# Kernel tuning notes

Hardware: AMD Instinct MI355X
Metric: run time of the kernel (lower is better)

The kernel has to match this reference:

```python
import jax, jax.numpy as jnp
import numpy as np

N = 100_000      # n_nodes
E = 1_000_000    # n_edges (avg degree 10)
DIN = 64
DOUT = 64


def setup_inputs() -> dict:
    key = jax.random.key(0)
    k1, k2, k3, k4 = jax.random.split(key, 4)
    x = jax.random.normal(k1, (N, DIN), dtype=jnp.float32)
    edge_index = jax.random.randint(k2, (2, E), 0, N, dtype=jnp.int32)
    # GCNConv linear weight (glorot-ish scale) and bias
    W = jax.random.normal(k3, (DIN, DOUT), dtype=jnp.float32) * (1.0 / np.sqrt(DIN))
    b = jax.random.normal(k4, (DOUT,), dtype=jnp.float32) * 0.01
    return {"x": x, "edge_index": edge_index, "W": W, "b": b}


def reference(x, edge_index, W, b):
    n = x.shape[0]
    # linear transform first (PyG GCNConv: x = self.lin(x))
    h = x @ W  # [N, DOUT]
    # add self-loops
    loop = jnp.arange(n, dtype=edge_index.dtype)
    row = jnp.concatenate([edge_index[0], loop])  # source j
    col = jnp.concatenate([edge_index[1], loop])  # target i
    # symmetric normalization: deg computed on target index (PyG gcn_norm)
    deg = jax.ops.segment_sum(jnp.ones(row.shape[0], dtype=h.dtype), col, num_segments=n)
    dinv = jnp.where(deg > 0, jax.lax.rsqrt(deg), 0.0)
    norm = dinv[row] * dinv[col]  # [E+N]
    # gather source features, scale, scatter-add to targets
    out = jax.ops.segment_sum(norm[:, None] * h[row], col, num_segments=n)
    out = out + b
    # dropout is identity in eval mode; act = relu
    return jax.nn.relu(out)
```

## Files before the change

kernel.cpp:

```cpp
#include <hip/hip_runtime.h>
#include <hip/hip_bf16.h>

#define F 64
#define BK 128
#define CAP 4096
#define ECAP 2048
#define PA_BLOCKS 256

typedef __attribute__((ext_vector_type(8))) short bf16x8;
typedef __attribute__((ext_vector_type(4))) float f32x4;

static __device__ inline short f2bf_bits(float f) {
    union { __hip_bfloat16 b; short s; } cv;
    cv.b = __float2bfloat16(f);
    return cv.s;
}

__global__ void __launch_bounds__(256)
passA_kernel(const int* __restrict__ row, const int* __restrict__ col,
             int* __restrict__ bcursor, unsigned* __restrict__ bin,
             int e, int K, int chunk) {
    __shared__ int lh[1024];
    __shared__ int lbase[1024];
    int tid = threadIdx.x;
    int s = blockIdx.x * chunk;
    int lim = min(s + chunk, e);
    for (int i = tid; i < K; i += 256) lh[i] = 0;
    __syncthreads();
    for (int i = s + tid; i < lim; i += 256) atomicAdd(&lh[col[i] >> 7], 1);
    __syncthreads();
    for (int i = tid; i < K; i += 256) {
        int c = lh[i];
        lbase[i] = c ? atomicAdd(&bcursor[i], c) : 0;
        lh[i] = 0;
    }
    __syncthreads();
    for (int i = s + tid; i < lim; i += 256) {
        int d = col[i];
        int bkt = d >> 7;
        int off = lbase[bkt] + atomicAdd(&lh[bkt], 1);
        if (off < CAP)
            bin[(size_t)bkt * CAP + off] = ((unsigned)row[i] << 7) | ((unsigned)d & 127u);
    }
}

__global__ void __launch_bounds__(256)
k2_kernel(const float* __restrict__ x, const float* __restrict__ W,
          __hip_bfloat16* __restrict__ h,
          const unsigned* __restrict__ bin, const int* __restrict__ bcursor,
          float* __restrict__ dinv, int n, int ngemm) {
    __shared__ short Wb[F * F];
    __shared__ int lcnt[BK];
    int tid = threadIdx.x;

    if ((int)blockIdx.x < ngemm) {
        for (int i = tid; i < F * F; i += 256) Wb[i] = f2bf_bits(W[i]);
        __syncthreads();
        int lane = tid & 63;
        int wv = tid >> 6;
        int quad = lane >> 4;
        int l16 = lane & 15;

        bf16x8 bfr[2][4];
#pragma unroll
        for (int ks = 0; ks < 2; ++ks)
#pragma unroll
            for (int nb = 0; nb < 4; ++nb) {
                bf16x8 f;
#pragma unroll
                for (int j = 0; j < 8; ++j)
                    f[j] = Wb[(ks * 32 + quad * 8 + j) * F + nb * 16 + l16];
                bfr[ks][nb] = f;
            }

        int blockbase = blockIdx.x * 256;
#pragma unroll
        for (int mt = 0; mt < 4; ++mt) {
            int trow = blockbase + (wv * 4 + mt) * 16;
            int ar = trow + l16;
            bf16x8 af0, af1;
            if (ar < n) {
                const float* xr = x + (size_t)ar * F + quad * 8;
                float4 v0 = ((const float4*)xr)[0];
                float4 v1 = ((const float4*)xr)[1];
                float4 v2 = ((const float4*)(xr + 32))[0];
                float4 v3 = ((const float4*)(xr + 32))[1];
                af0[0] = f2bf_bits(v0.x); af0[1] = f2bf_bits(v0.y);
                af0[2] = f2bf_bits(v0.z); af0[3] = f2bf_bits(v0.w);
                af0[4] = f2bf_bits(v1.x); af0[5] = f2bf_bits(v1.y);
                af0[6] = f2bf_bits(v1.z); af0[7] = f2bf_bits(v1.w);
                af1[0] = f2bf_bits(v2.x); af1[1] = f2bf_bits(v2.y);
                af1[2] = f2bf_bits(v2.z); af1[3] = f2bf_bits(v2.w);
                af1[4] = f2bf_bits(v3.x); af1[5] = f2bf_bits(v3.y);
                af1[6] = f2bf_bits(v3.z); af1[7] = f2bf_bits(v3.w);
            } else {
                af0 = (bf16x8)0; af1 = (bf16x8)0;
            }
            f32x4 acc[4];
#pragma unroll
            for (int nb = 0; nb < 4; ++nb) {
                acc[nb] = (f32x4)0.f;
                acc[nb] = __builtin_amdgcn_mfma_f32_16x16x32_bf16(af0, bfr[0][nb], acc[nb], 0, 0, 0);
                acc[nb] = __builtin_amdgcn_mfma_f32_16x16x32_bf16(af1, bfr[1][nb], acc[nb], 0, 0, 0);
            }
#pragma unroll
            for (int nb = 0; nb < 4; ++nb)
#pragma unroll
                for (int r = 0; r < 4; ++r) {
                    int grow = trow + quad * 4 + r;
                    if (grow < n)
                        h[(size_t)grow * F + nb * 16 + l16] = __float2bfloat16(acc[nb][r]);
                }
        }
    } else {
        int b = blockIdx.x - ngemm;
        int s = b * CAP;
        int cnt = min(bcursor[b], ECAP);
        if (tid < BK) lcnt[tid] = 0;
        __syncthreads();
        for (int p = tid; p < cnt; p += 256) atomicAdd(&lcnt[bin[s + p] & 127u], 1);
        __syncthreads();
        if (tid < BK) {
            int node = (b << 7) + tid;
            if (node < n) dinv[node] = rsqrtf((float)(lcnt[tid] + 1));
        }
    }
}

__global__ void __launch_bounds__(256)
gather_kernel(const unsigned* __restrict__ bin, const int* __restrict__ bcursor,
              const float* __restrict__ dinv, const __hip_bfloat16* __restrict__ h,
              const float* __restrict__ bias, float* __restrict__ out, int n) {
    __shared__ unsigned ebuf[ECAP];
    __shared__ int2 spair[ECAP];
    __shared__ int lcnt[BK];
    __shared__ int sstart[BK];
    __shared__ int lcur[BK];
    __shared__ int sc[BK];
    __shared__ float sdinv[BK];
    int tid = threadIdx.x;
    int b = blockIdx.x;
    int base = b << 7;
    int s = b * CAP;
    int cnt = min(bcursor[b], ECAP);

    if (tid < BK) lcnt[tid] = 0;
    __syncthreads();
    for (int p = tid; p < cnt; p += 256) {
        unsigned u = bin[s + p];
        ebuf[p] = u;
        atomicAdd(&lcnt[u & 127u], 1);
    }
    __syncthreads();
    if (tid < BK) sc[tid] = lcnt[tid];
    __syncthreads();
    for (int off = 1; off < BK; off <<= 1) {
        int t = (tid < BK && tid >= off) ? sc[tid - off] : 0;
        __syncthreads();
        if (tid < BK) sc[tid] += t;
        __syncthreads();
    }
    if (tid < BK) {
        int c = lcnt[tid];
        int st = sc[tid] - c;
        sstart[tid] = st;
        lcur[tid] = st;
        sdinv[tid] = rsqrtf((float)(c + 1));
    }
    __syncthreads();
    for (int p = tid; p < cnt; p += 256) {
        unsigned u = ebuf[p];
        int src = (int)(u >> 7);
        float w = dinv[src];
        int pos = atomicAdd(&lcur[u & 127u], 1);
        spair[pos] = make_int2(src, __float_as_int(w));
    }
    __syncthreads();

    int g = tid >> 3, cl = tid & 7;
    const uint4* h8 = (const uint4*)h;
#pragma unroll
    for (int r = 0; r < 4; ++r) {
        int ln = r * 32 + g;
        int node = base + ln;
        if (node >= n) continue;
        float di = sdinv[ln];
        float a0, a1, a2, a3, a4, a5, a6, a7;
        {
            uint4 hv = h8[(size_t)node * 8 + cl];
            a0 = di * __uint_as_float(hv.x << 16);
            a1 = di * __uint_as_float(hv.x & 0xffff0000u);
            a2 = di * __uint_as_float(hv.y << 16);
            a3 = di * __uint_as_float(hv.y & 0xffff0000u);
            a4 = di * __uint_as_float(hv.z << 16);
            a5 = di * __uint_as_float(hv.z & 0xffff0000u);
            a6 = di * __uint_as_float(hv.w << 16);
            a7 = di * __uint_as_float(hv.w & 0xffff0000u);
        }
        int p = sstart[ln];
        int pend = p + lcnt[ln];
        for (; p + 2 <= pend; p += 2) {
            int2 e0 = spair[p];
            int2 e1 = spair[p + 1];
            uint4 h0 = h8[(size_t)e0.x * 8 + cl];
            uint4 h1 = h8[(size_t)e1.x * 8 + cl];
            float w0 = __int_as_float(e0.y);
            float w1 = __int_as_float(e1.y);
            a0 += w0 * __uint_as_float(h0.x << 16);
            a1 += w0 * __uint_as_float(h0.x & 0xffff0000u);
            a2 += w0 * __uint_as_float(h0.y << 16);
            a3 += w0 * __uint_as_float(h0.y & 0xffff0000u);
            a4 += w0 * __uint_as_float(h0.z << 16);
            a5 += w0 * __uint_as_float(h0.z & 0xffff0000u);
            a6 += w0 * __uint_as_float(h0.w << 16);
            a7 += w0 * __uint_as_float(h0.w & 0xffff0000u);
            a0 += w1 * __uint_as_float(h1.x << 16);
            a1 += w1 * __uint_as_float(h1.x & 0xffff0000u);
            a2 += w1 * __uint_as_float(h1.y << 16);
            a3 += w1 * __uint_as_float(h1.y & 0xffff0000u);
            a4 += w1 * __uint_as_float(h1.z << 16);
            a5 += w1 * __uint_as_float(h1.z & 0xffff0000u);
            a6 += w1 * __uint_as_float(h1.w << 16);
            a7 += w1 * __uint_as_float(h1.w & 0xffff0000u);
        }
        if (p < pend) {
            int2 e0 = spair[p];
            uint4 h0 = h8[(size_t)e0.x * 8 + cl];
            float w0 = __int_as_float(e0.y);
            a0 += w0 * __uint_as_float(h0.x << 16);
            a1 += w0 * __uint_as_float(h0.x & 0xffff0000u);
            a2 += w0 * __uint_as_float(h0.y << 16);
            a3 += w0 * __uint_as_float(h0.y & 0xffff0000u);
            a4 += w0 * __uint_as_float(h0.z << 16);
            a5 += w0 * __uint_as_float(h0.z & 0xffff0000u);
            a6 += w0 * __uint_as_float(h0.w << 16);
            a7 += w0 * __uint_as_float(h0.w & 0xffff0000u);
        }
        float4 b0 = ((const float4*)bias)[cl * 2];
        float4 b1 = ((const float4*)bias)[cl * 2 + 1];
        float4 r0, r1;
        r0.x = di * a0 + b0.x; r0.y = di * a1 + b0.y;
        r0.z = di * a2 + b0.z; r0.w = di * a3 + b0.w;
        r1.x = di * a4 + b1.x; r1.y = di * a5 + b1.y;
        r1.z = di * a6 + b1.z; r1.w = di * a7 + b1.w;
        r0.x = r0.x > 0.f ? r0.x : 0.f; r0.y = r0.y > 0.f ? r0.y : 0.f;
        r0.z = r0.z > 0.f ? r0.z : 0.f; r0.w = r0.w > 0.f ? r0.w : 0.f;
        r1.x = r1.x > 0.f ? r1.x : 0.f; r1.y = r1.y > 0.f ? r1.y : 0.f;
        r1.z = r1.z > 0.f ? r1.z : 0.f; r1.w = r1.w > 0.f ? r1.w : 0.f;
        ((float4*)out)[(size_t)node * 16 + cl * 2] = r0;
        ((float4*)out)[(size_t)node * 16 + cl * 2 + 1] = r1;
    }
}

extern "C" void kernel_launch(void* const* d_in, const int* in_sizes, int n_in,
                              void* d_out, int out_size, void* d_ws, size_t ws_size,
                              hipStream_t stream) {
    const float* x = (const float*)d_in[0];
    const int* ei  = (const int*)d_in[1];
    const float* W = (const float*)d_in[2];
    const float* b = (const float*)d_in[3];
    float* out = (float*)d_out;

    int n = in_sizes[0] / F;
    int e = in_sizes[1] / 2;
    const int* row = ei;
    const int* col = ei + e;
    int K = (n + BK - 1) / BK;

    __hip_bfloat16* h = (__hip_bfloat16*)d_ws;
    unsigned* bin = (unsigned*)((char*)d_ws + (size_t)n * F * 2);
    float* dinv   = (float*)(bin + (size_t)K * CAP);
    int* bcursor  = (int*)(dinv + n);

    hipMemsetAsync(bcursor, 0, 1024 * sizeof(int), stream);

    int chunk = (e + PA_BLOCKS - 1) / PA_BLOCKS;
    passA_kernel<<<PA_BLOCKS, 256, 0, stream>>>(row, col, bcursor, bin, e, K, chunk);

    int ngemm = (n + 255) / 256;
    k2_kernel<<<ngemm + K, 256, 0, stream>>>(x, W, h, bin, bcursor, dinv, n, ngemm);

    gather_kernel<<<K, 256, 0, stream>>>(bin, bcursor, dinv, h, b, out, n);
}
```

Before: 143.8 us.

## Fuse GEMM, binning and degree count into one kernel; halve bucket size

Merges the bucket-binning pass, the bf16 MFMA GEMM and a new global-atomic degree count into a single launch, removing one kernel boundary and the separate dinv pass. The gather kernel now computes source normalisation from the raw degree array with rsqrt instead of loading a precomputed dinv. Buckets shrink from 128 to 64 nodes, doubling the number of gather blocks and halving per-block shared-memory buffers. The cost is heavy global atomics on deg, extra rsqrt work per edge, and a per-bucket edge cap that is halved, which may truncate high-degree buckets.

```diff
diff --git a/kernel.cpp b/kernel.cpp
--- a/kernel.cpp
+++ b/kernel.cpp
@@ -2,10 +2,11 @@
 #include <hip/hip_bf16.h>
 
 #define F 64
-#define BK 128
-#define CAP 4096
-#define ECAP 2048
+#define BK 64
+#define CAP 2048
+#define ECAP 1024
 #define PA_BLOCKS 256
+#define DC_BLOCKS 128
 
 typedef __attribute__((ext_vector_type(8))) short bf16x8;
 typedef __attribute__((ext_vector_type(4))) float f32x4;
@@ -17,43 +18,17 @@
 }
 
 __global__ void __launch_bounds__(256)
-passA_kernel(const int* __restrict__ row, const int* __restrict__ col,
-             int* __restrict__ bcursor, unsigned* __restrict__ bin,
-             int e, int K, int chunk) {
-    __shared__ int lh[1024];
-    __shared__ int lbase[1024];
+d1_kernel(const float* __restrict__ x, const float* __restrict__ W,
+          __hip_bfloat16* __restrict__ h,
+          const int* __restrict__ row, const int* __restrict__ col,
+          int* __restrict__ bcursor, unsigned* __restrict__ bin,
+          int* __restrict__ deg, int n, int e, int ngemm, int K, int chunk) {
+    __shared__ int smem[4096];
     int tid = threadIdx.x;
-    int s = blockIdx.x * chunk;
-    int lim = min(s + chunk, e);
-    for (int i = tid; i < K; i += 256) lh[i] = 0;
-    __syncthreads();
-    for (int i = s + tid; i < lim; i += 256) atomicAdd(&lh[col[i] >> 7], 1);
-    __syncthreads();
-    for (int i = tid; i < K; i += 256) {
-        int c = lh[i];
-        lbase[i] = c ? atomicAdd(&bcursor[i], c) : 0;
-        lh[i] = 0;
-    }
-    __syncthreads();
-    for (int i = s + tid; i < lim; i += 256) {
-        int d = col[i];
-        int bkt = d >> 7;
-        int off = lbase[bkt] + atomicAdd(&lh[bkt], 1);
-        if (off < CAP)
-            bin[(size_t)bkt * CAP + off] = ((unsigned)row[i] << 7) | ((unsigned)d & 127u);
-    }
-}
-
-__global__ void __launch_bounds__(256)
-k2_kernel(const float* __restrict__ x, const float* __restrict__ W,
-          __hip_bfloat16* __restrict__ h,
-          const unsigned* __restrict__ bin, const int* __restrict__ bcursor,
-          float* __restrict__ dinv, int n, int ngemm) {
-    __shared__ short Wb[F * F];
-    __shared__ int lcnt[BK];
-    int tid = threadIdx.x;
-
-    if ((int)blockIdx.x < ngemm) {
+    int bid = blockIdx.x;
+
+    if (bid < ngemm) {
+        short* Wb = (short*)smem;
         for (int i = tid; i < F * F; i += 256) Wb[i] = f2bf_bits(W[i]);
         __syncthreads();
         int lane = tid & 63;
@@ -73,7 +48,7 @@
                 bfr[ks][nb] = f;
             }
 
-        int blockbase = blockIdx.x * 256;
+        int blockbase = bid * 256;
 #pragma unroll
         for (int mt = 0; mt < 4; ++mt) {
             int trow = blockbase + (wv * 4 + mt) * 16;
@@ -112,24 +87,50 @@
                         h[(size_t)grow * F + nb * 16 + l16] = __float2bfloat16(acc[nb][r]);
                 }
         }
+    } else if (bid < ngemm + PA_BLOCKS) {
+        int* lh = smem;
+        int* lbase = smem + 2048;
+        int pb = bid - ngemm;
+        int s = pb * chunk;
+        int lim = min(s + chunk, e);
+        for (int i = tid; i < K; i += 256) lh[i] = 0;
+        __syncthreads();
+        for (int i = s + tid; i < lim; i += 256) atomicAdd(&lh[col[i] >> 6], 1);
+        __syncthreads();
+        for (int i = tid; i < K; i += 256) {
+            int c = lh[i];
+            lbase[i] = c ? atomicAdd(&bcursor[i], c) : 0;
+            lh[i] = 0;
+        }
+        __syncthreads();
+        for (int i = s + tid; i < lim; i += 256) {
+            int d = col[i];
+            int bkt = d >> 6;
+            int off = lbase[bkt] + atomicAdd(&lh[bkt], 1);
+            if (off < CAP)
+                bin[(size_t)bkt * CAP + off] = ((unsigned)row[i] << 6) | ((unsigned)d & 63u);
+        }
     } else {
-        int b = blockIdx.x - ngemm;
-        int s = b * CAP;
-        int cnt = min(bcursor[b], ECAP);
-        if (tid < BK) lcnt[tid] = 0;
-        __syncthreads();
-        for (int p = tid; p < cnt; p += 256) atomicAdd(&lcnt[bin[s + p] & 127u], 1);
-        __syncthreads();
-        if (tid < BK) {
-            int node = (b << 7) + tid;
-            if (node < n) dinv[node] = rsqrtf((float)(lcnt[tid] + 1));
+        int db = bid - ngemm - PA_BLOCKS;
+        int nv = e >> 2;
+        const int4* col4 = (const int4*)col;
+        int stride = DC_BLOCKS * 256;
+        for (int v = db * 256 + tid; v < nv; v += stride) {
+            int4 cs = col4[v];
+            atomicAdd(&deg[cs.x], 1);
+            atomicAdd(&deg[cs.y], 1);
+            atomicAdd(&deg[cs.z], 1);
+            atomicAdd(&deg[cs.w], 1);
+        }
+        if (db == 0 && tid == 0) {
+            for (int i = nv << 2; i < e; ++i) atomicAdd(&deg[col[i]], 1);
         }
     }
 }
 
 __global__ void __launch_bounds__(256)
 gather_kernel(const unsigned* __restrict__ bin, const int* __restrict__ bcursor,
-              const float* __restrict__ dinv, const __hip_bfloat16* __restrict__ h,
+              const int* __restrict__ deg, const __hip_bfloat16* __restrict__ h,
               const float* __restrict__ bias, float* __restrict__ out, int n) {
     __shared__ unsigned ebuf[ECAP];
     __shared__ int2 spair[ECAP];
@@ -140,8 +141,8 @@
     __shared__ float sdinv[BK];
     int tid = threadIdx.x;
     int b = blockIdx.x;
-    int base = b << 7;
-    int s = b * CAP;
+    int base = b << 6;
+    size_t s = (size_t)b * CAP;
     int cnt = min(bcursor[b], ECAP);
 
     if (tid < BK) lcnt[tid] = 0;
@@ -149,7 +150,7 @@
     for (int p = tid; p < cnt; p += 256) {
         unsigned u = bin[s + p];
         ebuf[p] = u;
-        atomicAdd(&lcnt[u & 127u], 1);
+        atomicAdd(&lcnt[u & 63u], 1);
     }
     __syncthreads();
     if (tid < BK) sc[tid] = lcnt[tid];
@@ -170,9 +171,9 @@
     __syncthreads();
     for (int p = tid; p < cnt; p += 256) {
         unsigned u = ebuf[p];
-        int src = (int)(u >> 7);
-        float w = dinv[src];
-        int pos = atomicAdd(&lcur[u & 127u], 1);
+        int src = (int)(u >> 6);
+        float w = rsqrtf((float)(deg[src] + 1));
+        int pos = atomicAdd(&lcur[u & 63u], 1);
         spair[pos] = make_int2(src, __float_as_int(w));
     }
     __syncthreads();
@@ -180,7 +181,7 @@
     int g = tid >> 3, cl = tid & 7;
     const uint4* h8 = (const uint4*)h;
 #pragma unroll
-    for (int r = 0; r < 4; ++r) {
+    for (int r = 0; r < 2; ++r) {
         int ln = r * 32 + g;
         int node = base + ln;
         if (node >= n) continue;
@@ -269,16 +270,15 @@
 
     __hip_bfloat16* h = (__hip_bfloat16*)d_ws;
     unsigned* bin = (unsigned*)((char*)d_ws + (size_t)n * F * 2);
-    float* dinv   = (float*)(bin + (size_t)K * CAP);
-    int* bcursor  = (int*)(dinv + n);
-
-    hipMemsetAsync(bcursor, 0, 1024 * sizeof(int), stream);
-
+    int* deg      = (int*)(bin + (size_t)K * CAP);
+    int* bcursor  = deg + n;
+
+    hipMemsetAsync(deg, 0, ((size_t)n + 2048) * sizeof(int), stream);
+
+    int ngemm = (n + 255) / 256;
     int chunk = (e + PA_BLOCKS - 1) / PA_BLOCKS;
-    passA_kernel<<<PA_BLOCKS, 256, 0, stream>>>(row, col, bcursor, bin, e, K, chunk);
-
-    int ngemm = (n + 255) / 256;
-    k2_kernel<<<ngemm + K, 256, 0, stream>>>(x, W, h, bin, bcursor, dinv, n, ngemm);
-
-    gather_kernel<<<K, 256, 0, stream>>>(bin, bcursor, dinv, h, b, out, n);
-}
+    d1_kernel<<<ngemm + PA_BLOCKS + DC_BLOCKS, 256, 0, stream>>>(
+        x, W, h, row, col, bcursor, bin, deg, n, e, ngemm, K, chunk);
+
+    gather_kernel<<<K, 256, 0, stream>>>(bin, bcursor, deg, h, b, out, n);
+}
```

New measurement: 164.7 us. +14.5%, slower.
